# Performance work log

Hardware: AMD Instinct MI355X
Metric: run time of the kernel (lower is better)

Reference implementation:

```python
import jax, jax.numpy as jnp
import numpy as np

B, C, H, W, N, NH, DFF = 2, 256, 128, 128, 8, 8, 1024
EPS = 1e-5


def _ln(x, g, b):
    m = jnp.mean(x, -1, keepdims=True)
    v = jnp.mean((x - m) ** 2, -1, keepdims=True)
    return (x - m) / jnp.sqrt(v + EPS) * g + b


def _mha(q, k, v, Wqkv, bqkv, Wo, bo, nh):
    # q,k,v: [Bq, S, C]; torch MultiheadAttention with packed in_proj
    Bq, S, Cd = q.shape
    dh = Cd // nh
    Wq, Wk, Wv = jnp.split(Wqkv, 3, axis=0)
    bq, bk, bv = jnp.split(bqkv, 3, axis=0)
    qp = (q @ Wq.T + bq).reshape(Bq, S, nh, dh).transpose(0, 2, 1, 3)
    kp = (k @ Wk.T + bk).reshape(Bq, S, nh, dh).transpose(0, 2, 1, 3)
    vp = (v @ Wv.T + bv).reshape(Bq, S, nh, dh).transpose(0, 2, 1, 3)
    scores = jnp.einsum('bhqd,bhkd->bhqk', qp, kp) / jnp.sqrt(jnp.asarray(dh, qp.dtype))
    attn = jax.nn.softmax(scores, axis=-1)
    o = jnp.einsum('bhqk,bhkd->bhqd', attn, vp).transpose(0, 2, 1, 3).reshape(Bq, S, Cd)
    return o @ Wo.T + bo


def _enc_layer(q, k, v, Wqkv, bqkv, Wo, bo, W1, b1, W2, b2, g1, be1, g2, be2, nh):
    # normalize_before=False, dropout=0
    src = _ln(v + _mha(q, k, v, Wqkv, bqkv, Wo, bo, nh), g1, be1)
    ffn = jax.nn.relu(src @ W1.T + b1) @ W2.T + b2
    return _ln(src + ffn, g2, be2)


def _encode(feat, pe, layer_params, nh):
    # feat: [Nv, hw, C]; pe = glob_pos + rel_pos broadcast: [Nv, hw, C]
    out = feat
    qk = out + pe
    out = _enc_layer(qk, qk, out, *layer_params, nh)
    out_t = out.transpose(1, 0, 2)                 # [hw, Nv, C] axis-permuted pass
    qk = out_t + pe.transpose(1, 0, 2)
    out = _enc_layer(qk, qk, out_t, *layer_params, nh).transpose(1, 0, 2)
    return out


def _forward(backbone_memory, defe_feature_filtered, glob_pos_embed,
             Wqkv, bqkv, Wo, bo, W1, b1, W2, b2, g1, be1, g2, be2,
             relW1, relb1, relW2, relb2, n):
    Bm, Cd, Hf, Wf = backbone_memory.shape
    h, w = Hf // n, Wf // n
    Nv, hw = n * n, h * w

    # relative position embedding: MLP over normalized grid coords [h,w,2]
    gy, gx = jnp.meshgrid(jnp.arange(h, dtype=jnp.float32),
                          jnp.arange(w, dtype=jnp.float32), indexing='ij')
    coords = jnp.stack([gx / (w - 1), gy / (h - 1)], axis=-1)
    rel = (jax.nn.relu(coords @ relW1.T + relb1) @ relW2.T + relb2)  # [h,w,C]
    rel = rel.reshape(1, hw, Cd)                                      # [1,hw,C]

    # window partition: [B, Nv, hw, C]
    win = backbone_memory.reshape(Bm, Cd, n, h, n, w).transpose(0, 2, 4, 1, 3, 5)
    win = win.reshape(Bm, Nv, Cd, hw).transpose(0, 1, 3, 2)

    # per-window global pos embed: [Nv, hw, C]
    glob = glob_pos_embed.reshape(Cd, n, h, n, w).transpose(1, 3, 0, 2, 4)
    glob = glob.reshape(Nv, Cd, hw).transpose(0, 2, 1)

    pe = glob + rel
    layer_params = (Wqkv, bqkv, Wo, bo, W1, b1, W2, b2, g1, be1, g2, be2)
    enc = jax.vmap(lambda f: _encode(f, pe, layer_params, NH))(win)   # [B,Nv,hw,C]

    # scatter windows back and add residually (reconstructed += feats)
    back = enc.transpose(0, 1, 3, 2).reshape(Bm, n, n, Cd, h, w)
    back = back.transpose(0, 3, 1, 4, 2, 5).reshape(Bm, Cd, Hf, Wf)
    reconstructed = backbone_memory + back

    # defe_mask via non-overlapping max-pool (all-ones mask -> all valid)
    Hm, Wm = defe_feature_filtered.shape[-2:]
    kh = (Hm // Hf) * h
    kw = (Wm // Wf) * w
    pooled = defe_feature_filtered.reshape(Bm, 1, n, kh, n, kw).max(axis=(3, 5))
    defe_mask = pooled[:, 0] > 0
    return reconstructed, defe_mask


def setup_inputs() -> dict:
    key = jax.random.key(0)
    ks = jax.random.split(key, 10)
    s = 0.02
    return {
        'backbone_memory': jax.random.normal(ks[0], (B, C, H, W), jnp.float32),
        'defe_feature_filtered': jnp.ones((B, 1, H, W), jnp.float32),
        'glob_pos_embed': jax.random.normal(ks[1], (C, H, W), jnp.float32),
        'Wqkv': jax.random.normal(ks[2], (3 * C, C), jnp.float32) * s,
        'bqkv': jnp.zeros((3 * C,), jnp.float32),
        'Wo': jax.random.normal(ks[3], (C, C), jnp.float32) * s,
        'bo': jnp.zeros((C,), jnp.float32),
        'W1': jax.random.normal(ks[4], (DFF, C), jnp.float32) * s,
        'b1': jnp.zeros((DFF,), jnp.float32),
        'W2': jax.random.normal(ks[5], (C, DFF), jnp.float32) * s,
        'b2': jnp.zeros((C,), jnp.float32),
        'g1': jnp.ones((C,), jnp.float32),
        'be1': jnp.zeros((C,), jnp.float32),
        'g2': jnp.ones((C,), jnp.float32),
        'be2': jnp.zeros((C,), jnp.float32),
        'relW1': jax.random.normal(ks[6], (64, 2), jnp.float32) * s,
        'relb1': jnp.zeros((64,), jnp.float32),
        'relW2': jax.random.normal(ks[7], (C, 64), jnp.float32) * s,
        'relb2': jnp.zeros((C,), jnp.float32),
        'n': N,
    }


def reference(backbone_memory, defe_feature_filtered, glob_pos_embed,
              Wqkv, bqkv, Wo, bo, W1, b1, W2, b2, g1, be1, g2, be2,
              relW1, relb1, relW2, relb2, n):
    return _forward(backbone_memory, defe_feature_filtered, glob_pos_embed,
                    Wqkv, bqkv, Wo, bo, W1, b1, W2, b2, g1, be1, g2, be2,
                    relW1, relb1, relW2, relb2, n)
```

## Files before the change

### kernel.cpp

```cpp
#include <hip/hip_runtime.h>
#include <hip/hip_bf16.h>

#define C_DIM 256
#define NHEAD 8
#define DH 32
#define NTOK 32768
#define PETOK 16384
#define DFF_DIM 1024
#define LN_EPS 1e-5f

typedef unsigned int u32;
typedef unsigned short ushortT;
using frag_ab = __attribute__((ext_vector_type(8))) short;
using f32x4   = __attribute__((ext_vector_type(4))) float;

__device__ __forceinline__ float bflo(u32 u) { union { u32 i; float f; } c; c.i = u << 16; return c.f; }
__device__ __forceinline__ float bfhi(u32 u) { union { u32 i; float f; } c; c.i = u & 0xffff0000u; return c.f; }
__device__ __forceinline__ float b2f(ushortT u) { union { u32 i; float f; } c; c.i = ((u32)u) << 16; return c.f; }
__device__ __forceinline__ ushortT f2b(float f) {
    __hip_bfloat16 b = __float2bfloat16(f);
    return *reinterpret_cast<ushortT*>(&b);
}
__device__ __forceinline__ u32 packbf(float lo, float hi) {
    float2 f2 = {lo, hi};
    __hip_bfloat162 h = __float22bfloat162_rn(f2);
    return *reinterpret_cast<u32*>(&h);
}
__device__ __forceinline__ void gload_lds16(const ushortT* g, ushortT* l) {
    __builtin_amdgcn_global_load_lds((const __attribute__((address_space(1))) void*)g,
                                     (__attribute__((address_space(3))) void*)l, 16, 0, 0);
}

__global__ void cvt_all_kernel(const float* __restrict__ Wqkv, const float* __restrict__ Wo,
                               const float* __restrict__ W1, const float* __restrict__ W2,
                               ushortT* __restrict__ dst) {
    const int i = (blockIdx.x * 256 + threadIdx.x) * 4;
    const float* src;
    int off;
    if (i < 196608)      { src = Wqkv; off = 0; }
    else if (i < 262144) { src = Wo;   off = 196608; }
    else if (i < 524288) { src = W1;   off = 262144; }
    else                 { src = W2;   off = 524288; }
    const float4 v = *(const float4*)&src[i - off];
    uint2 o = {packbf(v.x, v.y), packbf(v.z, v.w)};
    *(uint2*)&dst[i] = o;
}

__global__ __launch_bounds__(256) void pe_kernel(const float* __restrict__ glob,
                                                 const float* __restrict__ relW1,
                                                 const float* __restrict__ relb1,
                                                 const float* __restrict__ relW2,
                                                 const float* __restrict__ relb2,
                                                 ushortT* __restrict__ peb) {
    __shared__ float tile[32][129];
    __shared__ float relv[16][33];
    const int y = blockIdx.x;
    const int c0 = blockIdx.y * 32;
    const int i = y >> 4, ty = y & 15;
    const int tid = threadIdx.x;
    const int xl = tid & 127;
    #pragma unroll
    for (int p = 0; p < 16; ++p) {
        const int cl = p * 2 + (tid >> 7);
        tile[cl][xl] = glob[(size_t)(c0 + cl) * 16384 + y * 128 + xl];
    }
    const float cy = ty * (1.0f / 15.0f);
    #pragma unroll
    for (int p = 0; p < 2; ++p) {
        const int idx = p * 256 + tid;
        const int tl = idx >> 5;
        const int cl = idx & 31;
        const float cx = tl * (1.0f / 15.0f);
        float acc = relb2[c0 + cl];
        #pragma unroll 8
        for (int j = 0; j < 64; ++j) {
            const float hh = fmaxf(relW1[j * 2] * cx + relW1[j * 2 + 1] * cy + relb1[j], 0.0f);
            acc = fmaf(hh, relW2[(c0 + cl) * 64 + j], acc);
        }
        relv[tl][cl] = acc;
    }
    __syncthreads();
    const int cl = tid & 31;
    #pragma unroll
    for (int p = 0; p < 16; ++p) {
        const int x = p * 8 + (tid >> 5);
        const int v = i * 8 + (x >> 4);
        const int t = ty * 16 + (x & 15);
        const float val = tile[cl][x] + relv[x & 15][cl];
        peb[(size_t)(v * 256 + t) * C_DIM + c0 + cl] = f2b(val);
    }
}

__global__ __launch_bounds__(256) void window_kernel(const float* __restrict__ backbone,
                                                     const ushortT* __restrict__ peb,
                                                     ushortT* __restrict__ Xb,
                                                     ushortT* __restrict__ XPEb) {
    __shared__ float tile[32][129];
    const int y = blockIdx.x;
    const int c0 = blockIdx.y * 32;
    const int b = blockIdx.z;
    const int i = y >> 4, ty = y & 15;
    const int tid = threadIdx.x;
    const int xl = tid & 127;
    #pragma unroll
    for (int p = 0; p < 16; ++p) {
        const int cl = p * 2 + (tid >> 7);
        tile[cl][xl] = backbone[(size_t)b * 4194304 + (size_t)(c0 + cl) * 16384 + y * 128 + xl];
    }
    __syncthreads();
    const int cl = tid & 31;
    #pragma unroll
    for (int p = 0; p < 16; ++p) {
        const int x = p * 8 + (tid >> 5);
        const int v = i * 8 + (x >> 4);
        const int t = ty * 16 + (x & 15);
        const size_t vt = (size_t)(v * 256 + t);
        const size_t tok = (size_t)b * PETOK + vt;
        const float val = tile[cl][x];
        Xb[tok * C_DIM + c0 + cl] = f2b(val);
        XPEb[tok * C_DIM + c0 + cl] = f2b(val + b2f(peb[vt * C_DIM + c0 + cl]));
    }
}

__global__ __launch_bounds__(256) void scatter_kernel(const float* __restrict__ backbone,
                                                      const ushortT* __restrict__ X,
                                                      float* __restrict__ out) {
    __shared__ ushortT tile[128][34];
    const int y = blockIdx.x;
    const int c0 = blockIdx.y * 32;
    const int b = blockIdx.z;
    const int i = y >> 4, ty = y & 15;
    const int tid = threadIdx.x;
    const int cl = tid & 31;
    #pragma unroll
    for (int p = 0; p < 16; ++p) {
        const int x = p * 8 + (tid >> 5);
        const int v = i * 8 + (x >> 4);
        const int t = ty * 16 + (x & 15);
        const size_t tok = (size_t)b * PETOK + v * 256 + t;
        tile[x][cl] = X[tok * C_DIM + c0 + cl];
    }
    __syncthreads();
    const int xl = tid & 127;
    #pragma unroll
    for (int p = 0; p < 16; ++p) {
        const int c = c0 + p * 2 + (tid >> 7);
        const size_t gi = (size_t)b * 4194304 + (size_t)c * 16384 + y * 128 + xl;
        out[gi] = backbone[gi] + b2f(tile[xl][p * 2 + (tid >> 7)]);
    }
}

#define BM 128
#define BN 128
#define BK 32

template<bool QKVMODE, bool RELU>
__global__ __launch_bounds__(256) void gemm_bf16(
        const ushortT* __restrict__ A,
        const ushortT* __restrict__ A2,
        int lda,
        const ushortT* __restrict__ W,
        const float* __restrict__ bias,
        ushortT* __restrict__ Cout, int ldc, int K) {
    __shared__ ushortT As[2][BM][BK];
    __shared__ ushortT Bs[2][BN][BK];
    const int nwg = gridDim.x * gridDim.y;
    const int flat = blockIdx.y * gridDim.x + blockIdx.x;
    const int cpx = nwg >> 3;
    const int swz = (flat & 7) * cpx + (flat >> 3);
    const int m0 = (swz / gridDim.x) * BM;
    const int n0 = (swz % gridDim.x) * BN;
    const ushortT* Ause = (QKVMODE && n0 >= 512) ? A2 : A;
    const int tid = threadIdx.x;
    const int lane = tid & 63;
    const int wave = tid >> 6;
    const int wm = (wave >> 1) * 64;
    const int wn = (wave & 1) * 64;
    const int fr = lane & 15;
    const int fg = lane >> 4;
    const int gRow = wave * 32 + (lane >> 2);
    const int gCol = (lane & 3) * 8;

    f32x4 acc[4][4];
    #pragma unroll
    for (int i = 0; i < 4; ++i)
        #pragma unroll
        for (int j = 0; j < 4; ++j)
            acc[i][j] = (f32x4){0.f, 0.f, 0.f, 0.f};

    for (int k0 = 0; k0 < K; k0 += 2 * BK) {
        #pragma unroll
        for (int kk = 0; kk < 2; ++kk) {
            const int kb = k0 + kk * BK;
            gload_lds16(&Ause[(size_t)(m0 + gRow) * lda + kb + gCol], &As[kk][wave * 32][0]);
            gload_lds16(&Ause[(size_t)(m0 + gRow + 16) * lda + kb + gCol], &As[kk][wave * 32 + 16][0]);
            gload_lds16(&W[(size_t)(n0 + gRow) * K + kb + gCol], &Bs[kk][wave * 32][0]);
            gload_lds16(&W[(size_t)(n0 + gRow + 16) * K + kb + gCol], &Bs[kk][wave * 32 + 16][0]);
        }
        __syncthreads();
        #pragma unroll
        for (int kk = 0; kk < 2; ++kk) {
            frag_ab af[4], bf[4];
            #pragma unroll
            for (int i = 0; i < 4; ++i) af[i] = *(const frag_ab*)&As[kk][wm + i * 16 + fr][fg * 8];
            #pragma unroll
            for (int j = 0; j < 4; ++j) bf[j] = *(const frag_ab*)&Bs[kk][wn + j * 16 + fr][fg * 8];
            #pragma unroll
            for (int i = 0; i < 4; ++i)
                #pragma unroll
                for (int j = 0; j < 4; ++j)
                    acc[i][j] = __builtin_amdgcn_mfma_f32_16x16x32_bf16(af[i], bf[j], acc[i][j], 0, 0, 0);
        }
        __syncthreads();
    }
    #pragma unroll
    for (int j = 0; j < 4; ++j) {
        const int n = n0 + wn + j * 16 + fr;
        const float bv = bias[n];
        #pragma unroll
        for (int i = 0; i < 4; ++i) {
            const int mb = m0 + wm + i * 16 + fg * 4;
            #pragma unroll
            for (int r2 = 0; r2 < 2; ++r2) {
                float a0 = acc[i][j][2 * r2] + bv;
                float a1 = acc[i][j][2 * r2 + 1] + bv;
                if (RELU) { a0 = fmaxf(a0, 0.0f); a1 = fmaxf(a1, 0.0f); }
                const u32 u = packbf(a0, a1);
                Cout[(size_t)(mb + 2 * r2) * ldc + n] = (ushortT)u;
                Cout[(size_t)(mb + 2 * r2 + 1) * ldc + n] = (ushortT)(u >> 16);
            }
        }
    }
}

#define KVC 128
__global__ __launch_bounds__(256) void attn_p0(const ushortT* __restrict__ QKVb,
                                               ushortT* __restrict__ Ob) {
    __shared__ ushortT K_lds[KVC * 40];
    __shared__ ushortT V_t[32 * 136];
    __shared__ ushortT P_lds[4][16 * 136];
    const int grp = blockIdx.x;
    const int h = grp & 7;
    const int bv = grp >> 3;
    const int base = (bv >> 6) * PETOK + (bv & 63) * 256;
    const int tid = threadIdx.x;
    const int wave = tid >> 6;
    const int lane = tid & 63;
    const int fr = lane & 15;
    const int fg = lane >> 4;
    const float scale = 0.17677669529663687f;

    frag_ab qf[4];
    size_t qtok[4];
    #pragma unroll
    for (int s = 0; s < 4; ++s) {
        qtok[s] = (size_t)(base + wave * 64 + s * 16 + fr);
        qf[s] = *(const frag_ab*)&QKVb[qtok[s] * 768 + h * DH + fg * 8];
    }
    float m[4], l[4];
    f32x4 o0[4], o1[4];
    #pragma unroll
    for (int s = 0; s < 4; ++s) {
        m[s] = -1e30f; l[s] = 0.f;
        o0[s] = (f32x4){0.f, 0.f, 0.f, 0.f};
        o1[s] = (f32x4){0.f, 0.f, 0.f, 0.f};
    }

    for (int c = 0; c < 2; ++c) {
        __syncthreads();
        #pragma unroll
        for (int it = 0; it < 2; ++it) {
            const int idx = it * 256 + tid;
            const int row = idx >> 2, ch = idx & 3;
            const size_t tok = (size_t)(base + c * KVC + row);
            const uint4 kv = *(const uint4*)&QKVb[tok * 768 + 256 + h * DH + ch * 8];
            *(uint4*)&K_lds[row * 40 + ch * 8] = kv;
            const uint4 vv = *(const uint4*)&QKVb[tok * 768 + 512 + h * DH + ch * 8];
            const ushortT* vp = (const ushortT*)&vv;
            #pragma unroll
            for (int e = 0; e < 8; ++e) V_t[(ch * 8 + e) * 136 + row] = vp[e];
        }
        __syncthreads();
        #pragma unroll
        for (int s = 0; s < 4; ++s) {
            f32x4 sc[8];
            #pragma unroll
            for (int kt = 0; kt < 8; ++kt) {
                const frag_ab kf = *(const frag_ab*)&K_lds[(kt * 16 + fr) * 40 + fg * 8];
                sc[kt] = __builtin_amdgcn_mfma_f32_16x16x32_bf16(kf, qf[s], (f32x4){0.f, 0.f, 0.f, 0.f}, 0, 0, 0);
            }
            float mx = -1e30f;
            #pragma unroll
            for (int kt = 0; kt < 8; ++kt)
                mx = fmaxf(mx, fmaxf(fmaxf(sc[kt][0], sc[kt][1]), fmaxf(sc[kt][2], sc[kt][3])));
            mx = fmaxf(mx, __shfl_xor(mx, 16, 64));
            mx = fmaxf(mx, __shfl_xor(mx, 32, 64));
            const float nm = fmaxf(m[s], mx);
            const float corr = __expf((m[s] - nm) * scale);
            m[s] = nm;
            float lsum = 0.f;
            #pragma unroll
            for (int kt = 0; kt < 8; ++kt) {
                const float p0 = __expf((sc[kt][0] - nm) * scale);
                const float p1 = __expf((sc[kt][1] - nm) * scale);
                const float p2 = __expf((sc[kt][2] - nm) * scale);
                const float p3 = __expf((sc[kt][3] - nm) * scale);
                lsum += (p0 + p1) + (p2 + p3);
                uint2 pk;
                pk.x = packbf(p0, p1);
                pk.y = packbf(p2, p3);
                *(uint2*)&P_lds[wave][fr * 136 + kt * 16 + fg * 4] = pk;
            }
            lsum += __shfl_xor(lsum, 16, 64);
            lsum += __shfl_xor(lsum, 32, 64);
            l[s] = l[s] * corr + lsum;
            o0[s] *= corr;
            o1[s] *= corr;
            #pragma unroll
            for (int kc = 0; kc < 4; ++kc) {
                const frag_ab pf = *(const frag_ab*)&P_lds[wave][fr * 136 + kc * 32 + fg * 8];
                const frag_ab v0 = *(const frag_ab*)&V_t[fr * 136 + kc * 32 + fg * 8];
                const frag_ab v1 = *(const frag_ab*)&V_t[(16 + fr) * 136 + kc * 32 + fg * 8];
                o0[s] = __builtin_amdgcn_mfma_f32_16x16x32_bf16(v0, pf, o0[s], 0, 0, 0);
                o1[s] = __builtin_amdgcn_mfma_f32_16x16x32_bf16(v1, pf, o1[s], 0, 0, 0);
            }
        }
    }
    #pragma unroll
    for (int s = 0; s < 4; ++s) {
        const float inv = 1.0f / l[s];
        ushortT* ob = &Ob[qtok[s] * C_DIM + h * DH];
        uint2 w0, w1;
        w0.x = packbf(o0[s][0] * inv, o0[s][1] * inv);
        w0.y = packbf(o0[s][2] * inv, o0[s][3] * inv);
        w1.x = packbf(o1[s][0] * inv, o1[s][1] * inv);
        w1.y = packbf(o1[s][2] * inv, o1[s][3] * inv);
        *(uint2*)&ob[fg * 4] = w0;
        *(uint2*)&ob[16 + fg * 4] = w1;
    }
}

__global__ __launch_bounds__(256) void attn_p1(const ushortT* __restrict__ QKVb,
                                               ushortT* __restrict__ Ob) {
    __shared__ ushortT K_lds[4][64 * 40];
    __shared__ ushortT V_t[4][32 * 72];
    __shared__ ushortT P_lds[4][16 * 72];
    const int wave = threadIdx.x >> 6;
    const int lane = threadIdx.x & 63;
    const int unit = blockIdx.x * 4 + wave;
    const int h = unit & 7;
    const int g = unit >> 3;
    const int base = (g >> 8) * PETOK + (g & 255);
    const int fr = lane & 15;
    const int fg = lane >> 4;
    const float scale = 0.17677669529663687f;
    #pragma unroll
    for (int it = 0; it < 4; ++it) {
        const int idx = it * 64 + lane;
        const int row = idx >> 2, ch = idx & 3;
        const size_t tok = (size_t)(base + row * 256);
        const uint4 kv = *(const uint4*)&QKVb[tok * 768 + 256 + h * DH + ch * 8];
        *(uint4*)&K_lds[wave][row * 40 + ch * 8] = kv;
        const uint4 vv = *(const uint4*)&QKVb[tok * 768 + 512 + h * DH + ch * 8];
        const ushortT* vp = (const ushortT*)&vv;
        #pragma unroll
        for (int e = 0; e < 8; ++e) V_t[wave][(ch * 8 + e) * 72 + row] = vp[e];
    }
    #pragma unroll
    for (int s = 0; s < 4; ++s) {
        const int qq = s * 16 + fr;
        const size_t qtok = (size_t)(base + qq * 256);
        const frag_ab qf = *(const frag_ab*)&QKVb[qtok * 768 + h * DH + fg * 8];
        f32x4 sc[4];
        #pragma unroll
        for (int kt = 0; kt < 4; ++kt) {
            const frag_ab kf = *(const frag_ab*)&K_lds[wave][(kt * 16 + fr) * 40 + fg * 8];
            sc[kt] = __builtin_amdgcn_mfma_f32_16x16x32_bf16(kf, qf, (f32x4){0.f, 0.f, 0.f, 0.f}, 0, 0, 0);
        }
        float mx = -1e30f;
        #pragma unroll
        for (int kt = 0; kt < 4; ++kt)
            mx = fmaxf(mx, fmaxf(fmaxf(sc[kt][0], sc[kt][1]), fmaxf(sc[kt][2], sc[kt][3])));
        mx = fmaxf(mx, __shfl_xor(mx, 16, 64));
        mx = fmaxf(mx, __shfl_xor(mx, 32, 64));
        float lsum = 0.f;
        #pragma unroll
        for (int kt = 0; kt < 4; ++kt) {
            const float p0 = __expf((sc[kt][0] - mx) * scale);
            const float p1 = __expf((sc[kt][1] - mx) * scale);
            const float p2 = __expf((sc[kt][2] - mx) * scale);
            const float p3 = __expf((sc[kt][3] - mx) * scale);
            lsum += (p0 + p1) + (p2 + p3);
            uint2 pk;
            pk.x = packbf(p0, p1);
            pk.y = packbf(p2, p3);
            *(uint2*)&P_lds[wave][fr * 72 + kt * 16 + fg * 4] = pk;
        }
        lsum += __shfl_xor(lsum, 16, 64);
        lsum += __shfl_xor(lsum, 32, 64);
        f32x4 o0 = {0.f, 0.f, 0.f, 0.f}, o1 = {0.f, 0.f, 0.f, 0.f};
        #pragma unroll
        for (int kc = 0; kc < 2; ++kc) {
            const frag_ab pf = *(const frag_ab*)&P_lds[wave][fr * 72 + kc * 32 + fg * 8];
            const frag_ab v0 = *(const frag_ab*)&V_t[wave][fr * 72 + kc * 32 + fg * 8];
            const frag_ab v1 = *(const frag_ab*)&V_t[wave][(16 + fr) * 72 + kc * 32 + fg * 8];
            o0 = __builtin_amdgcn_mfma_f32_16x16x32_bf16(v0, pf, o0, 0, 0, 0);
            o1 = __builtin_amdgcn_mfma_f32_16x16x32_bf16(v1, pf, o1, 0, 0, 0);
        }
        const float inv = 1.0f / lsum;
        ushortT* ob = &Ob[qtok * C_DIM + h * DH];
        uint2 w0, w1;
        w0.x = packbf(o0[0] * inv, o0[1] * inv);
        w0.y = packbf(o0[2] * inv, o0[3] * inv);
        w1.x = packbf(o1[0] * inv, o1[1] * inv);
        w1.y = packbf(o1[2] * inv, o1[3] * inv);
        *(uint2*)&ob[fg * 4] = w0;
        *(uint2*)&ob[16 + fg * 4] = w1;
    }
}

template<bool WXPE>
__global__ __launch_bounds__(256) void ln_kernel(ushortT* __restrict__ X, const ushortT* __restrict__ Y,
                                                 const float* __restrict__ g, const float* __restrict__ be,
                                                 const ushortT* __restrict__ peb,
                                                 ushortT* __restrict__ XPE) {
    int tok = blockIdx.x * 4 + (threadIdx.x >> 6);
    int lane = threadIdx.x & 63;
    const uint2 xu = *(const uint2*)&X[(size_t)tok * C_DIM + lane * 4];
    const uint2 yu = *(const uint2*)&Y[(size_t)tok * C_DIM + lane * 4];
    float v0 = bflo(xu.x) + bflo(yu.x), v1 = bfhi(xu.x) + bfhi(yu.x);
    float v2 = bflo(xu.y) + bflo(yu.y), v3 = bfhi(xu.y) + bfhi(yu.y);
    float s = v0 + v1 + v2 + v3;
    float ss = v0 * v0 + v1 * v1 + v2 * v2 + v3 * v3;
    #pragma unroll
    for (int off = 32; off; off >>= 1) {
        s += __shfl_xor(s, off, 64);
        ss += __shfl_xor(ss, off, 64);
    }
    float mean = s * (1.0f / 256.0f);
    float var = ss * (1.0f / 256.0f) - mean * mean;
    float inv = rsqrtf(var + LN_EPS);
    const float4 gv = *(const float4*)&g[lane * 4];
    const float4 bv = *(const float4*)&be[lane * 4];
    float o0 = (v0 - mean) * inv * gv.x + bv.x;
    float o1 = (v1 - mean) * inv * gv.y + bv.y;
    float o2 = (v2 - mean) * inv * gv.z + bv.z;
    float o3 = (v3 - mean) * inv * gv.w + bv.w;
    uint2 ob = {packbf(o0, o1), packbf(o2, o3)};
    *(uint2*)&X[(size_t)tok * C_DIM + lane * 4] = ob;
    if (WXPE) {
        const size_t vt = (size_t)(tok & 16383);
        const uint2 pu = *(const uint2*)&peb[vt * C_DIM + lane * 4];
        uint2 xp;
        xp.x = packbf(o0 + bflo(pu.x), o1 + bfhi(pu.x));
        xp.y = packbf(o2 + bflo(pu.y), o3 + bfhi(pu.y));
        *(uint2*)&XPE[(size_t)tok * C_DIM + lane * 4] = xp;
    }
}

__global__ void mask_kernel(const float* __restrict__ defe, float* __restrict__ out) {
    __shared__ float wmax[4];
    const int idx = blockIdx.x;
    const int b = idx >> 6;
    const int ii = (idx >> 3) & 7;
    const int jj = idx & 7;
    const int t = threadIdx.x;
    const int y = t >> 4, xx = t & 15;
    float v = defe[b * 16384 + (ii * 16 + y) * 128 + jj * 16 + xx];
    #pragma unroll
    for (int off = 32; off; off >>= 1) v = fmaxf(v, __shfl_xor(v, off, 64));
    if ((t & 63) == 0) wmax[t >> 6] = v;
    __syncthreads();
    if (t == 0) {
        float mx = fmaxf(fmaxf(wmax[0], wmax[1]), fmaxf(wmax[2], wmax[3]));
        out[8388608 + idx] = (mx > 0.0f) ? 1.0f : 0.0f;
    }
}

extern "C" void kernel_launch(void* const* d_in, const int* in_sizes, int n_in,
                              void* d_out, int out_size, void* d_ws, size_t ws_size,
                              hipStream_t stream) {
    const float* backbone = (const float*)d_in[0];
    const float* defe     = (const float*)d_in[1];
    const float* glob     = (const float*)d_in[2];
    const float* Wqkv     = (const float*)d_in[3];
    const float* bqkv     = (const float*)d_in[4];
    const float* Wo       = (const float*)d_in[5];
    const float* bo       = (const float*)d_in[6];
    const float* W1       = (const float*)d_in[7];
    const float* b1       = (const float*)d_in[8];
    const float* W2       = (const float*)d_in[9];
    const float* b2       = (const float*)d_in[10];
    const float* g1       = (const float*)d_in[11];
    const float* be1      = (const float*)d_in[12];
    const float* g2       = (const float*)d_in[13];
    const float* be2      = (const float*)d_in[14];
    const float* relW1    = (const float*)d_in[15];
    const float* relb1    = (const float*)d_in[16];
    const float* relW2    = (const float*)d_in[17];
    const float* relb2    = (const float*)d_in[18];

    ushortT* peb    = (ushortT*)d_ws;
    ushortT* Wqkv_b = peb + 4194304;
    ushortT* Wo_b   = Wqkv_b + 196608;
    ushortT* W1_b   = Wo_b + 65536;
    ushortT* W2_b   = W1_b + 262144;
    ushortT* Xb     = W2_b + 262144;
    ushortT* XPEb   = Xb + 8388608;
    ushortT* QKVb   = XPEb + 8388608;
    ushortT* Ob     = QKVb + 25165824;
    ushortT* Hb     = QKVb;
    ushortT* Yb     = Ob + 8388608;
    size_t needed = (size_t)((char*)(Yb + 8388608) - (char*)d_ws);
    if (ws_size < needed) return;

    cvt_all_kernel<<<768, 256, 0, stream>>>(Wqkv, Wo, W1, W2, Wqkv_b);
    pe_kernel<<<dim3(128, 8), 256, 0, stream>>>(glob, relW1, relb1, relW2, relb2, peb);
    window_kernel<<<dim3(128, 8, 2), 256, 0, stream>>>(backbone, peb, Xb, XPEb);

    for (int pass = 0; pass < 2; ++pass) {
        gemm_bf16<true, false><<<dim3(768 / BN, NTOK / BM), 256, 0, stream>>>(
            XPEb, Xb, C_DIM, Wqkv_b, bqkv, QKVb, 768, C_DIM);
        if (pass == 0) {
            attn_p0<<<128 * NHEAD, 256, 0, stream>>>(QKVb, Ob);
        } else {
            attn_p1<<<4096 / 4, 256, 0, stream>>>(QKVb, Ob);
        }
        gemm_bf16<false, false><<<dim3(256 / BN, NTOK / BM), 256, 0, stream>>>(
            Ob, nullptr, C_DIM, Wo_b, bo, Yb, C_DIM, C_DIM);
        ln_kernel<false><<<NTOK / 4, 256, 0, stream>>>(Xb, Yb, g1, be1, nullptr, nullptr);
        gemm_bf16<false, true><<<dim3(DFF_DIM / BN, NTOK / BM), 256, 0, stream>>>(
            Xb, nullptr, C_DIM, W1_b, b1, Hb, DFF_DIM, C_DIM);
        gemm_bf16<false, false><<<dim3(256 / BN, NTOK / BM), 256, 0, stream>>>(
            Hb, nullptr, DFF_DIM, W2_b, b2, Yb, C_DIM, DFF_DIM);
        if (pass == 0) {
            ln_kernel<true><<<NTOK / 4, 256, 0, stream>>>(Xb, Yb, g2, be2, peb, XPEb);
        } else {
            ln_kernel<false><<<NTOK / 4, 256, 0, stream>>>(Xb, Yb, g2, be2, nullptr, nullptr);
        }
    }

    scatter_kernel<<<dim3(128, 8, 2), 256, 0, stream>>>(backbone, Xb, (float*)d_out);
    mask_kernel<<<128, 256, 0, stream>>>(defe, (float*)d_out);
}
```

Baseline: 346.7 us.

## Add 128x256 wide-tile GEMM for QKV and FFN1, single-stage K loop

```diff
diff --git a/kernel.cpp b/kernel.cpp
--- a/kernel.cpp
+++ b/kernel.cpp
@@ -154,23 +154,20 @@
 #define BN 128
 #define BK 32
 
-template<bool QKVMODE, bool RELU>
+template<bool RELU>
 __global__ __launch_bounds__(256) void gemm_bf16(
-        const ushortT* __restrict__ A,
-        const ushortT* __restrict__ A2,
-        int lda,
+        const ushortT* __restrict__ A, int lda,
         const ushortT* __restrict__ W,
         const float* __restrict__ bias,
         ushortT* __restrict__ Cout, int ldc, int K) {
-    __shared__ ushortT As[2][BM][BK];
-    __shared__ ushortT Bs[2][BN][BK];
+    __shared__ ushortT As[BM][BK];
+    __shared__ ushortT Bs[BN][BK];
     const int nwg = gridDim.x * gridDim.y;
     const int flat = blockIdx.y * gridDim.x + blockIdx.x;
     const int cpx = nwg >> 3;
     const int swz = (flat & 7) * cpx + (flat >> 3);
     const int m0 = (swz / gridDim.x) * BM;
     const int n0 = (swz % gridDim.x) * BN;
-    const ushortT* Ause = (QKVMODE && n0 >= 512) ? A2 : A;
     const int tid = threadIdx.x;
     const int lane = tid & 63;
     const int wave = tid >> 6;
@@ -188,29 +185,95 @@
         for (int j = 0; j < 4; ++j)
             acc[i][j] = (f32x4){0.f, 0.f, 0.f, 0.f};
 
-    for (int k0 = 0; k0 < K; k0 += 2 * BK) {
-        #pragma unroll
-        for (int kk = 0; kk < 2; ++kk) {
-            const int kb = k0 + kk * BK;
-            gload_lds16(&Ause[(size_t)(m0 + gRow) * lda + kb + gCol], &As[kk][wave * 32][0]);
-            gload_lds16(&Ause[(size_t)(m0 + gRow + 16) * lda + kb + gCol], &As[kk][wave * 32 + 16][0]);
-            gload_lds16(&W[(size_t)(n0 + gRow) * K + kb + gCol], &Bs[kk][wave * 32][0]);
-            gload_lds16(&W[(size_t)(n0 + gRow + 16) * K + kb + gCol], &Bs[kk][wave * 32 + 16][0]);
-        }
+    for (int k0 = 0; k0 < K; k0 += BK) {
+        gload_lds16(&A[(size_t)(m0 + gRow) * lda + k0 + gCol], &As[wave * 32][0]);
+        gload_lds16(&A[(size_t)(m0 + gRow + 16) * lda + k0 + gCol], &As[wave * 32 + 16][0]);
+        gload_lds16(&W[(size_t)(n0 + gRow) * K + k0 + gCol], &Bs[wave * 32][0]);
+        gload_lds16(&W[(size_t)(n0 + gRow + 16) * K + k0 + gCol], &Bs[wave * 32 + 16][0]);
         __syncthreads();
-        #pragma unroll
-        for (int kk = 0; kk < 2; ++kk) {
-            frag_ab af[4], bf[4];
-            #pragma unroll
-            for (int i = 0; i < 4; ++i) af[i] = *(const frag_ab*)&As[kk][wm + i * 16 + fr][fg * 8];
-            #pragma unroll
-            for (int j = 0; j < 4; ++j) bf[j] = *(const frag_ab*)&Bs[kk][wn + j * 16 + fr][fg * 8];
-            #pragma unroll
-            for (int i = 0; i < 4; ++i)
-                #pragma unroll
-                for (int j = 0; j < 4; ++j)
-                    acc[i][j] = __builtin_amdgcn_mfma_f32_16x16x32_bf16(af[i], bf[j], acc[i][j], 0, 0, 0);
-        }
+        frag_ab af[4], bf[4];
+        #pragma unroll
+        for (int i = 0; i < 4; ++i) af[i] = *(const frag_ab*)&As[wm + i * 16 + fr][fg * 8];
+        #pragma unroll
+        for (int j = 0; j < 4; ++j) bf[j] = *(const frag_ab*)&Bs[wn + j * 16 + fr][fg * 8];
+        #pragma unroll
+        for (int i = 0; i < 4; ++i)
+            #pragma unroll
+            for (int j = 0; j < 4; ++j)
+                acc[i][j] = __builtin_amdgcn_mfma_f32_16x16x32_bf16(af[i], bf[j], acc[i][j], 0, 0, 0);
+        __syncthreads();
+    }
+    #pragma unroll
+    for (int j = 0; j < 4; ++j) {
+        const int n = n0 + wn + j * 16 + fr;
+        const float bv = bias[n];
+        #pragma unroll
+        for (int i = 0; i < 4; ++i) {
+            const int mb = m0 + wm + i * 16 + fg * 4;
+            #pragma unroll
+            for (int r2 = 0; r2 < 2; ++r2) {
+                float a0 = acc[i][j][2 * r2] + bv;
+                float a1 = acc[i][j][2 * r2 + 1] + bv;
+                if (RELU) { a0 = fmaxf(a0, 0.0f); a1 = fmaxf(a1, 0.0f); }
+                const u32 u = packbf(a0, a1);
+                Cout[(size_t)(mb + 2 * r2) * ldc + n] = (ushortT)u;
+                Cout[(size_t)(mb + 2 * r2 + 1) * ldc + n] = (ushortT)(u >> 16);
+            }
+        }
+    }
+}
+
+#define WBN 256
+
+template<bool QKVMODE, bool RELU>
+__global__ __launch_bounds__(512) void gemm_wide(
+        const ushortT* __restrict__ A,
+        const ushortT* __restrict__ A2,
+        int lda,
+        const ushortT* __restrict__ W,
+        const float* __restrict__ bias,
+        ushortT* __restrict__ Cout, int ldc, int K) {
+    __shared__ ushortT As[BM][BK];
+    __shared__ ushortT Bs[WBN][BK];
+    const int nwg = gridDim.x * gridDim.y;
+    const int flat = blockIdx.y * gridDim.x + blockIdx.x;
+    const int cpx = nwg >> 3;
+    const int swz = (flat & 7) * cpx + (flat >> 3);
+    const int m0 = (swz / gridDim.x) * BM;
+    const int n0 = (swz % gridDim.x) * WBN;
+    const ushortT* Ause = (QKVMODE && n0 >= 512) ? A2 : A;
+    const int tid = threadIdx.x;
+    const int lane = tid & 63;
+    const int wave = tid >> 6;
+    const int wm = (wave >> 2) * 64;
+    const int wn = (wave & 3) * 64;
+    const int fr = lane & 15;
+    const int fg = lane >> 4;
+    const int gR = lane >> 2;
+    const int gC = (lane & 3) * 8;
+
+    f32x4 acc[4][4];
+    #pragma unroll
+    for (int i = 0; i < 4; ++i)
+        #pragma unroll
+        for (int j = 0; j < 4; ++j)
+            acc[i][j] = (f32x4){0.f, 0.f, 0.f, 0.f};
+
+    for (int k0 = 0; k0 < K; k0 += BK) {
+        gload_lds16(&Ause[(size_t)(m0 + wave * 16 + gR) * lda + k0 + gC], &As[wave * 16][0]);
+        gload_lds16(&W[(size_t)(n0 + wave * 32 + gR) * K + k0 + gC], &Bs[wave * 32][0]);
+        gload_lds16(&W[(size_t)(n0 + wave * 32 + 16 + gR) * K + k0 + gC], &Bs[wave * 32 + 16][0]);
+        __syncthreads();
+        frag_ab af[4], bf[4];
+        #pragma unroll
+        for (int i = 0; i < 4; ++i) af[i] = *(const frag_ab*)&As[wm + i * 16 + fr][fg * 8];
+        #pragma unroll
+        for (int j = 0; j < 4; ++j) bf[j] = *(const frag_ab*)&Bs[wn + j * 16 + fr][fg * 8];
+        #pragma unroll
+        for (int i = 0; i < 4; ++i)
+            #pragma unroll
+            for (int j = 0; j < 4; ++j)
+                acc[i][j] = __builtin_amdgcn_mfma_f32_16x16x32_bf16(af[i], bf[j], acc[i][j], 0, 0, 0);
         __syncthreads();
     }
     #pragma unroll
@@ -519,20 +582,20 @@
     window_kernel<<<dim3(128, 8, 2), 256, 0, stream>>>(backbone, peb, Xb, XPEb);
 
     for (int pass = 0; pass < 2; ++pass) {
-        gemm_bf16<true, false><<<dim3(768 / BN, NTOK / BM), 256, 0, stream>>>(
+        gemm_wide<true, false><<<dim3(768 / WBN, NTOK / BM), 512, 0, stream>>>(
             XPEb, Xb, C_DIM, Wqkv_b, bqkv, QKVb, 768, C_DIM);
         if (pass == 0) {
             attn_p0<<<128 * NHEAD, 256, 0, stream>>>(QKVb, Ob);
         } else {
             attn_p1<<<4096 / 4, 256, 0, stream>>>(QKVb, Ob);
         }
-        gemm_bf16<false, false><<<dim3(256 / BN, NTOK / BM), 256, 0, stream>>>(
-            Ob, nullptr, C_DIM, Wo_b, bo, Yb, C_DIM, C_DIM);
+        gemm_bf16<false><<<dim3(256 / BN, NTOK / BM), 256, 0, stream>>>(
+            Ob, C_DIM, Wo_b, bo, Yb, C_DIM, C_DIM);
         ln_kernel<false><<<NTOK / 4, 256, 0, stream>>>(Xb, Yb, g1, be1, nullptr, nullptr);
-        gemm_bf16<false, true><<<dim3(DFF_DIM / BN, NTOK / BM), 256, 0, stream>>>(
+        gemm_wide<false, true><<<dim3(DFF_DIM / WBN, NTOK / BM), 512, 0, stream>>>(
             Xb, nullptr, C_DIM, W1_b, b1, Hb, DFF_DIM, C_DIM);
-        gemm_bf16<false, false><<<dim3(256 / BN, NTOK / BM), 256, 0, stream>>>(
-            Hb, nullptr, DFF_DIM, W2_b, b2, Yb, C_DIM, DFF_DIM);
+        gemm_bf16<false><<<dim3(256 / BN, NTOK / BM), 256, 0, stream>>>(
+            Hb, DFF_DIM, W2_b, b2, Yb, C_DIM, DFF_DIM);
         if (pass == 0) {
             ln_kernel<true><<<NTOK / 4, 256, 0, stream>>>(Xb, Yb, g2, be2, peb, XPEb);
         } else {
```

After: 343.4 us. About the same (-1.0%).
